# Performance work log

Measured on AMD Instinct MI355X. Metric: run time of the kernel, lower is better.

Reference implementation:

```python
import jax, jax.numpy as jnp
import numpy as np


def setup_inputs() -> dict:
    key = jax.random.key(0)
    k1, k2 = jax.random.split(key)
    pred = jax.random.normal(k1, (4, 8192, 3), dtype=jnp.float32)
    target = jax.random.normal(k2, (4, 8192, 3), dtype=jnp.float32)
    return {"pred": pred, "target": target}


def reference(pred, target):
    # Pairwise squared distances via the expansion ||p-q||^2 = ||p||^2 + ||q||^2 - 2 p.q
    # Avoids materializing the O(B*M*N*3) diff tensor of the naive broadcast.
    p_sq = jnp.sum(pred * pred, axis=-1)          # [B, M]
    q_sq = jnp.sum(target * target, axis=-1)      # [B, N]
    cross = jnp.einsum("bmd,bnd->bmn", pred, target)  # [B, M, N]
    dist_sq = p_sq[:, :, None] + q_sq[:, None, :] - 2.0 * cross  # [B, M, N]
    min_dist_pred = jnp.min(dist_sq, axis=2).mean(axis=1)    # [B] min over target per pred point
    min_dist_target = jnp.min(dist_sq, axis=1).mean(axis=1)  # [B] min over pred per target point
    return jnp.mean(min_dist_pred + min_dist_target)
```

## Files before the change

kernel.cpp:

```cpp
#include <hip/hip_runtime.h>


#define THREADS 512
#define P 8
#define S 32
#define G 128
#define TILE 32
#define LSTRIDE (TILE + 1)
#define TSPLIT 2
#define BUFSZ (S * LSTRIDE)

typedef float float2_t __attribute__((ext_vector_type(2)));
typedef float float4_t __attribute__((ext_vector_type(4)));

__global__ __launch_bounds__(THREADS, 2) void chamfer_min_kernel(
    const float* __restrict__ pred, const float* __restrict__ target,
    float* __restrict__ wsmin, int M) {
  const int blocksPerDir = M / G;
  int bid = blockIdx.x;
  int pblk = bid % blocksPerDir;
  int rest = bid / blocksPerDir;
  int ts = rest % TSPLIT;
  int bd = rest / TSPLIT;
  int dir = bd & 1;
  int b = bd >> 1;
  const float* src = (dir ? target : pred) + (size_t)b * M * 3;
  const float* ref = (dir ? pred : target) + (size_t)b * M * 3;

  __shared__ float4_t lds[2 * BUFSZ];

  int t = threadIdx.x;
  int g = t >> 4;
  int l = t & 15;

  float ax[P], ay[P], az[P];
  int pbase = pblk * G;
#pragma unroll
  for (int i = 0; i < P; ++i) {
    int p = pbase + l + 16 * i;
    float x = src[p * 3 + 0], y = src[p * 3 + 1], z = src[p * 3 + 2];
    ax[i] = -2.f * x;
    ay[i] = -2.f * y;
    az[i] = -2.f * z;
  }
  float mn[P];
#pragma unroll
  for (int i = 0; i < P; ++i) mn[i] = 3.0e38f;

  const int spanLen = M / TSPLIT;
  const int tbase = ts * spanLen;
  const int sliceLen = spanLen / S;
  const int ntiles = sliceLen / TILE;

  const int sidx = 2 * t;
  const int ss = sidx >> 5;
  const int sjj = sidx & (TILE - 1);
  const int nb = tbase + ss * sliceLen + sjj;
  float rx0, ry0, rz0, rx1, ry1, rz1;

  {
    int n = nb;
    rx0 = ref[n * 3 + 0]; ry0 = ref[n * 3 + 1]; rz0 = ref[n * 3 + 2];
    rx1 = ref[n * 3 + 3]; ry1 = ref[n * 3 + 4]; rz1 = ref[n * 3 + 5];
    float4_t* dst = lds + ss * LSTRIDE + sjj;
    dst[0] = (float4_t){rx0, ry0, rz0, rx0 * rx0 + ry0 * ry0 + rz0 * rz0};
    dst[1] = (float4_t){rx1, ry1, rz1, rx1 * rx1 + ry1 * ry1 + rz1 * rz1};
  }
  __syncthreads();

  int cur = 0;
  for (int k = 0; k < ntiles; ++k) {
    if (k + 1 < ntiles) {
      int n = nb + (k + 1) * TILE;
      rx0 = ref[n * 3 + 0]; ry0 = ref[n * 3 + 1]; rz0 = ref[n * 3 + 2];
      rx1 = ref[n * 3 + 3]; ry1 = ref[n * 3 + 4]; rz1 = ref[n * 3 + 5];
    }
    const float4_t* tp = lds + cur * BUFSZ + g * LSTRIDE;
#pragma unroll 2
    for (int j = 0; j < TILE; j += 4) {
      float4_t q0 = tp[j + 0];
      float4_t q1 = tp[j + 1];
      float4_t q2 = tp[j + 2];
      float4_t q3 = tp[j + 3];
#pragma unroll
      for (int i = 0; i < P; ++i) {
        float d0 = fmaf(ax[i], q0.x, fmaf(ay[i], q0.y, fmaf(az[i], q0.z, q0.w)));
        float d1 = fmaf(ax[i], q1.x, fmaf(ay[i], q1.y, fmaf(az[i], q1.z, q1.w)));
        float d2 = fmaf(ax[i], q2.x, fmaf(ay[i], q2.y, fmaf(az[i], q2.z, q2.w)));
        float d3 = fmaf(ax[i], q3.x, fmaf(ay[i], q3.y, fmaf(az[i], q3.z, q3.w)));
        mn[i] = fminf(fminf(mn[i], d0), d1);
        mn[i] = fminf(fminf(mn[i], d2), d3);
      }
    }
    if (k + 1 < ntiles) {
      float4_t* dst = lds + (cur ^ 1) * BUFSZ + ss * LSTRIDE + sjj;
      dst[0] = (float4_t){rx0, ry0, rz0, rx0 * rx0 + ry0 * ry0 + rz0 * rz0};
      dst[1] = (float4_t){rx1, ry1, rz1, rx1 * rx1 + ry1 * ry1 + rz1 * rz1};
    }
    __syncthreads();
    cur ^= 1;
  }

  float* lmin = (float*)lds;
#pragma unroll
  for (int i = 0; i < P; ++i) {
    lmin[g * G + (l + 16 * i)] = mn[i];
  }
  __syncthreads();
  if (t < G) {
    float m = 3.0e38f;
#pragma unroll
    for (int s = 0; s < S; ++s) m = fminf(m, lmin[s * G + t]);
    int p = pbase + t;
    float x = src[p * 3 + 0], y = src[p * 3 + 1], z = src[p * 3 + 2];
    int pid = (b * 2 + dir) * M + p;
    wsmin[(size_t)pid * TSPLIT + ts] = (x * x + y * y + z * z) + m;
  }
}

__global__ __launch_bounds__(256) void chamfer_reduce_kernel(
    const float* __restrict__ wsmin, float* __restrict__ out, int npts,
    float scale) {
  int tid = blockIdx.x * blockDim.x + threadIdx.x;
  int stride = gridDim.x * blockDim.x;
  double acc = 0.0;
  for (int p = tid; p < npts; p += stride) {
    float2_t v = ((const float2_t*)wsmin)[p];
    acc += (double)fminf(v.x, v.y);
  }
  for (int off = 32; off > 0; off >>= 1) acc += __shfl_down(acc, off, 64);
  __shared__ double wsum[256 / 64];
  int t = threadIdx.x;
  if ((t & 63) == 0) wsum[t >> 6] = acc;
  __syncthreads();
  if (t == 0) {
    double s = 0.0;
#pragma unroll
    for (int w = 0; w < 256 / 64; ++w) s += wsum[w];
    atomicAdd(out, (float)(s * (double)scale));
  }
}

extern "C" void kernel_launch(void* const* d_in, const int* in_sizes, int n_in,
                              void* d_out, int out_size, void* d_ws,
                              size_t ws_size, hipStream_t stream) {
  const float* pred = (const float*)d_in[0];
  const float* target = (const float*)d_in[1];
  float* out = (float*)d_out;
  float* wsmin = (float*)d_ws;
  const int B = 4;
  const int M = in_sizes[0] / (B * 3);

  float scale = 1.0f / (float)(B * M);

  hipMemsetAsync(out, 0, sizeof(float), stream);
  int blocks = B * 2 * (M / G) * TSPLIT;
  chamfer_min_kernel<<<blocks, THREADS, 0, stream>>>(pred, target, wsmin, M);
  int npts = B * 2 * M;
  chamfer_reduce_kernel<<<64, 256, 0, stream>>>(wsmin, out, npts, scale);
}
```

Baseline: 101.0 us.

## Bin points along x and prune nearest-neighbor search by slab distance

A new pre-pass counting-sorts each point cloud into 256 x-bins and stores xyz plus squared norm as float4. The main kernel then gives each block a spatially coherent group of 128 sorted points. It loads reference bins outward from that group's x-range in tiles of 512, and stops once the block's worst current nearest distance is no larger than the squared x-gap to the next unvisited bin. This removes most of the all-pairs distance work. In exchange it adds a serial-ish sort kernel, tile loads with a barrier each round and no double buffering, and a block index that hardcodes 64 blocks per direction. The brute-force path is kept as a fallback when the workspace is too small.

```diff
diff --git a/kernel.cpp b/kernel.cpp
--- a/kernel.cpp
+++ b/kernel.cpp
@@ -3,17 +3,210 @@
 
 #define THREADS 512
 #define P 8
-#define S 32
 #define G 128
+#define NBINS 256
+#define XLO -6.0f
+#define XHI 6.0f
+#define TT 512
+#define LSTRIDE17 17
+#define MAXTILES 34
+
 #define TILE 32
 #define LSTRIDE (TILE + 1)
 #define TSPLIT 2
-#define BUFSZ (S * LSTRIDE)
+#define BUFSZ (32 * LSTRIDE)
 
 typedef float float2_t __attribute__((ext_vector_type(2)));
 typedef float float4_t __attribute__((ext_vector_type(4)));
 
+__global__ __launch_bounds__(THREADS) void bin_sort_kernel(
+    const float* __restrict__ pred, const float* __restrict__ target,
+    float4_t* __restrict__ sorted, int* __restrict__ binBase, int M) {
+  int bs = blockIdx.x;
+  int b = bs >> 1, side = bs & 1;
+  const float* src = (side ? target : pred) + (size_t)b * M * 3;
+  float4_t* out = sorted + (size_t)bs * M;
+  int* bases = binBase + bs * (NBINS + 1);
+
+  __shared__ int cnt[NBINS];
+  __shared__ int cur[NBINS];
+  int t = threadIdx.x;
+  for (int i = t; i < NBINS; i += THREADS) cnt[i] = 0;
+  __syncthreads();
+  const float invW = (float)NBINS / (XHI - XLO);
+  for (int i = t; i < M; i += THREADS) {
+    float x = src[i * 3];
+    int bin = (int)((x - XLO) * invW);
+    bin = bin < 0 ? 0 : (bin > NBINS - 1 ? NBINS - 1 : bin);
+    atomicAdd(&cnt[bin], 1);
+  }
+  __syncthreads();
+  if (t == 0) {
+    int acc = 0;
+    for (int i = 0; i < NBINS; ++i) {
+      int c = cnt[i];
+      cur[i] = acc;
+      bases[i] = acc;
+      acc += c;
+    }
+    bases[NBINS] = acc;
+  }
+  __syncthreads();
+  for (int i = t; i < M; i += THREADS) {
+    float x = src[i * 3], y = src[i * 3 + 1], z = src[i * 3 + 2];
+    int bin = (int)((x - XLO) * invW);
+    bin = bin < 0 ? 0 : (bin > NBINS - 1 ? NBINS - 1 : bin);
+    int pos = atomicAdd(&cur[bin], 1);
+    out[pos] = (float4_t){x, y, z, x * x + y * y + z * z};
+  }
+}
+
 __global__ __launch_bounds__(THREADS, 2) void chamfer_min_kernel(
+    const float4_t* __restrict__ sorted, const int* __restrict__ binBase,
+    float* __restrict__ wsmin, int M) {
+  int bid = blockIdx.x;
+  int pblk = bid & 63;
+  int bd = bid >> 6;
+  int dir = bd & 1, b = bd >> 1;
+  int srcBS = b * 2 + dir;
+  int refBS = b * 2 + (dir ^ 1);
+  const float4_t* src = sorted + (size_t)srcBS * M;
+  const float4_t* ref = sorted + (size_t)refBS * M;
+  const int* rbase = binBase + refBS * (NBINS + 1);
+
+  __shared__ float4_t shbuf[1024];
+  __shared__ float wred[THREADS / 64];
+  float4_t* tile = shbuf;
+
+  int t = threadIdx.x;
+  int g = t >> 4;
+  int l = t & 15;
+  int pbase = pblk * G;
+
+  float ax[P], ay[P], az[P], cm[P], mn[P];
+  float pxmn = 1e30f, pxmx = -1e30f;
+#pragma unroll
+  for (int i = 0; i < P; ++i) {
+    float4_t v = src[pbase + l + 16 * i];
+    ax[i] = -2.f * v.x;
+    ay[i] = -2.f * v.y;
+    az[i] = -2.f * v.z;
+    cm[i] = v.w;
+    mn[i] = 3.0e38f;
+    pxmn = fminf(pxmn, v.x);
+    pxmx = fmaxf(pxmx, v.x);
+  }
+  for (int off = 32; off > 0; off >>= 1) {
+    pxmn = fminf(pxmn, __shfl_xor(pxmn, off, 64));
+    pxmx = fmaxf(pxmx, __shfl_xor(pxmx, off, 64));
+  }
+
+  const float W = (XHI - XLO) / (float)NBINS;
+  const float invW = 1.0f / W;
+  int cl = (int)((pxmn - XLO) * invW);
+  cl = cl < 0 ? 0 : (cl > NBINS - 1 ? NBINS - 1 : cl);
+  int cr = cl + 1;
+  int offL = 0, offR = 0;
+
+  for (int iter = 0; iter < MAXTILES; ++iter) {
+    int filled = 0;
+    while (filled < TT && (cl >= 0 || cr < NBINS)) {
+      float gapL = (cl >= 0) ? fmaxf(0.f, pxmn - (XLO + (cl + 1) * W)) : 1e30f;
+      float gapR = (cr < NBINS) ? fmaxf(0.f, (XLO + cr * W) - pxmx) : 1e30f;
+      bool left = gapL <= gapR;
+      int bin = left ? cl : cr;
+      int beg = rbase[bin], end = rbase[bin + 1];
+      int cnt = end - beg;
+      int off = left ? offL : offR;
+      int avail = cnt - off;
+      int take = avail < (TT - filled) ? avail : (TT - filled);
+      for (int i = t; i < take; i += THREADS) {
+        int li = filled + i;
+        tile[(li >> 4) * LSTRIDE17 + (li & 15)] = ref[beg + off + i];
+      }
+      filled += take;
+      if (left) {
+        offL += take;
+        if (offL >= cnt) { cl--; offL = 0; }
+      } else {
+        offR += take;
+        if (offR >= cnt) { cr++; offR = 0; }
+      }
+    }
+    for (int i = filled + t; i < TT; i += THREADS) {
+      tile[(i >> 4) * LSTRIDE17 + (i & 15)] =
+          (float4_t){0.f, 0.f, 0.f, 3.0e38f};
+    }
+    __syncthreads();
+
+    const float4_t* tp = tile + g * LSTRIDE17;
+#pragma unroll 2
+    for (int j = 0; j < 16; j += 4) {
+      float4_t q0 = tp[j + 0];
+      float4_t q1 = tp[j + 1];
+      float4_t q2 = tp[j + 2];
+      float4_t q3 = tp[j + 3];
+#pragma unroll
+      for (int i = 0; i < P; ++i) {
+        float d0 = fmaf(ax[i], q0.x, fmaf(ay[i], q0.y, fmaf(az[i], q0.z, q0.w)));
+        float d1 = fmaf(ax[i], q1.x, fmaf(ay[i], q1.y, fmaf(az[i], q1.z, q1.w)));
+        float d2 = fmaf(ax[i], q2.x, fmaf(ay[i], q2.y, fmaf(az[i], q2.z, q2.w)));
+        float d3 = fmaf(ax[i], q3.x, fmaf(ay[i], q3.y, fmaf(az[i], q3.z, q3.w)));
+        mn[i] = fminf(fminf(mn[i], d0), d1);
+        mn[i] = fminf(fminf(mn[i], d2), d3);
+      }
+    }
+
+    float tmax = -1e30f;
+#pragma unroll
+    for (int i = 0; i < P; ++i) tmax = fmaxf(tmax, mn[i] + cm[i]);
+    for (int off = 32; off > 0; off >>= 1)
+      tmax = fmaxf(tmax, __shfl_xor(tmax, off, 64));
+    if ((t & 63) == 0) wred[t >> 6] = tmax;
+    __syncthreads();
+    float bm = fmaxf(fmaxf(fmaxf(wred[0], wred[1]), fmaxf(wred[2], wred[3])),
+                     fmaxf(fmaxf(wred[4], wred[5]), fmaxf(wred[6], wred[7])));
+    if (cl < 0 && cr >= NBINS) break;
+    float gapL = (cl >= 0) ? fmaxf(0.f, pxmn - (XLO + (cl + 1) * W)) : 1e30f;
+    float gapR = (cr < NBINS) ? fmaxf(0.f, (XLO + cr * W) - pxmx) : 1e30f;
+    float gg = fminf(gapL, gapR);
+    if (bm <= gg * gg * 0.999f) break;
+  }
+
+  float* lmin = (float*)shbuf;
+#pragma unroll
+  for (int i = 0; i < P; ++i) lmin[g * G + (l + 16 * i)] = mn[i];
+  __syncthreads();
+  if (t < G) {
+    float m = 3.0e38f;
+#pragma unroll
+    for (int s = 0; s < 32; ++s) m = fminf(m, lmin[s * G + t]);
+    float psq = src[pbase + t].w;
+    wsmin[(size_t)srcBS * M + pbase + t] = psq + m;
+  }
+}
+
+__global__ __launch_bounds__(256) void chamfer_reduce_kernel(
+    const float* __restrict__ wsmin, float* __restrict__ out, int npts,
+    float scale) {
+  int tid = blockIdx.x * blockDim.x + threadIdx.x;
+  int stride = gridDim.x * blockDim.x;
+  double acc = 0.0;
+  for (int p = tid; p < npts; p += stride) acc += (double)wsmin[p];
+  for (int off = 32; off > 0; off >>= 1) acc += __shfl_down(acc, off, 64);
+  __shared__ double wsum[256 / 64];
+  int t = threadIdx.x;
+  if ((t & 63) == 0) wsum[t >> 6] = acc;
+  __syncthreads();
+  if (t == 0) {
+    double s = 0.0;
+#pragma unroll
+    for (int w = 0; w < 256 / 64; ++w) s += wsum[w];
+    atomicAdd(out, (float)(s * (double)scale));
+  }
+}
+
+__global__ __launch_bounds__(THREADS, 2) void chamfer_brute_kernel(
     const float* __restrict__ pred, const float* __restrict__ target,
     float* __restrict__ wsmin, int M) {
   const int blocksPerDir = M / G;
@@ -49,7 +242,7 @@
 
   const int spanLen = M / TSPLIT;
   const int tbase = ts * spanLen;
-  const int sliceLen = spanLen / S;
+  const int sliceLen = spanLen / 32;
   const int ntiles = sliceLen / TILE;
 
   const int sidx = 2 * t;
@@ -103,14 +296,12 @@
 
   float* lmin = (float*)lds;
 #pragma unroll
-  for (int i = 0; i < P; ++i) {
-    lmin[g * G + (l + 16 * i)] = mn[i];
-  }
+  for (int i = 0; i < P; ++i) lmin[g * G + (l + 16 * i)] = mn[i];
   __syncthreads();
   if (t < G) {
     float m = 3.0e38f;
 #pragma unroll
-    for (int s = 0; s < S; ++s) m = fminf(m, lmin[s * G + t]);
+    for (int s = 0; s < 32; ++s) m = fminf(m, lmin[s * G + t]);
     int p = pbase + t;
     float x = src[p * 3 + 0], y = src[p * 3 + 1], z = src[p * 3 + 2];
     int pid = (b * 2 + dir) * M + p;
@@ -118,7 +309,7 @@
   }
 }
 
-__global__ __launch_bounds__(256) void chamfer_reduce_kernel(
+__global__ __launch_bounds__(256) void chamfer_reduce2_kernel(
     const float* __restrict__ wsmin, float* __restrict__ out, int npts,
     float scale) {
   int tid = blockIdx.x * blockDim.x + threadIdx.x;
@@ -147,15 +338,34 @@
   const float* pred = (const float*)d_in[0];
   const float* target = (const float*)d_in[1];
   float* out = (float*)d_out;
-  float* wsmin = (float*)d_ws;
   const int B = 4;
   const int M = in_sizes[0] / (B * 3);
-
   float scale = 1.0f / (float)(B * M);
 
   hipMemsetAsync(out, 0, sizeof(float), stream);
-  int blocks = B * 2 * (M / G) * TSPLIT;
-  chamfer_min_kernel<<<blocks, THREADS, 0, stream>>>(pred, target, wsmin, M);
-  int npts = B * 2 * M;
-  chamfer_reduce_kernel<<<64, 256, 0, stream>>>(wsmin, out, npts, scale);
-}
+
+  size_t needWsmin = (size_t)B * 2 * M * 4;
+  size_t needSorted = (size_t)B * 2 * M * 16;
+  size_t needBins = (size_t)B * 2 * (NBINS + 1) * 4;
+  size_t need = needWsmin + needSorted + needBins;
+
+  if (ws_size >= need) {
+    float* wsmin = (float*)d_ws;
+    float4_t* sorted = (float4_t*)((char*)d_ws + needWsmin);
+    int* binBase = (int*)((char*)sorted + needSorted);
+    bin_sort_kernel<<<B * 2, THREADS, 0, stream>>>(pred, target, sorted,
+                                                   binBase, M);
+    int blocks = B * 2 * (M / G);
+    chamfer_min_kernel<<<blocks, THREADS, 0, stream>>>(sorted, binBase, wsmin,
+                                                       M);
+    int npts = B * 2 * M;
+    chamfer_reduce_kernel<<<64, 256, 0, stream>>>(wsmin, out, npts, scale);
+  } else {
+    float* wsmin = (float*)d_ws;
+    int blocks = B * 2 * (M / G) * TSPLIT;
+    chamfer_brute_kernel<<<blocks, THREADS, 0, stream>>>(pred, target, wsmin,
+                                                         M);
+    int npts = B * 2 * M;
+    chamfer_reduce2_kernel<<<64, 256, 0, stream>>>(wsmin, out, npts, scale);
+  }
+}
```

After: 177.3 us. 75.5% more time.
